# Kernel optimization log

Measured on AMD Instinct MI355X. Metric: run time of the kernel, lower is better.

The kernel has to match this reference:

```python
import jax, jax.numpy as jnp
import numpy as np

BN_EPS = 1e-5


def _conv1x1(x, W, b):
    # x: (B, Cin, H, W), W: (Cout, Cin), b: (Cout,)
    return jnp.einsum('bchw,oc->bohw', x, W) + b[None, :, None, None]


def _bn(x, gamma, beta, mean, var):
    # inference-mode BatchNorm2d with running stats
    inv = gamma / jnp.sqrt(var + BN_EPS)
    return x * inv[None, :, None, None] + (beta - mean * inv)[None, :, None, None]


def setup_inputs() -> dict:
    key = jax.random.key(0)
    ks = jax.random.split(key, 8)
    B, N, C, H, W = 4, 3, 256, 48, 48
    Ck = C // 2  # key/query/value channels (scale=2)
    s = 0.02
    return {
        'x': jax.random.normal(ks[0], (B, N, C, H, W), jnp.float32),
        # f_key / f_query (shared): conv1x1 + BN
        'Wk': jax.random.normal(ks[1], (Ck, C), jnp.float32) * s,
        'bk': jnp.zeros((Ck,), jnp.float32),
        'gk': jnp.ones((Ck,), jnp.float32),
        'betak': jnp.zeros((Ck,), jnp.float32),
        'mk': jnp.zeros((Ck,), jnp.float32),
        'vk': jnp.ones((Ck,), jnp.float32),
        # f_value
        'Wv': jax.random.normal(ks[2], (Ck, C), jnp.float32) * s,
        'bv': jnp.zeros((Ck,), jnp.float32),
        # f_out
        'Wo': jax.random.normal(ks[3], (C, Ck), jnp.float32) * s,
        'bo': jnp.zeros((C,), jnp.float32),
        # fuse_layer: in = 2*C, out = C
        'Wf': jax.random.normal(ks[4], (C, 2 * C), jnp.float32) * s,
        'bf': jnp.zeros((C,), jnp.float32),
    }


def reference(x, Wk, bk, gk, betak, mk, vk, Wv, bv, Wo, bo, Wf, bf):
    B, N, C, H, W = x.shape  # N == 3
    HW = H * W
    Ck = Wk.shape[0]
    scale = Ck ** (-0.5)

    # Precompute shared key/query and value features for all 3 views
    xf = x.reshape(B * N, C, H, W)
    k_all = _bn(_conv1x1(xf, Wk, bk), gk, betak, mk, vk).reshape(B, N, Ck, HW)
    v_all = _conv1x1(xf, Wv, bv).reshape(B, N, Ck, HW)

    outs = []
    attn_maps = []
    for i in range(3):  # fixed small structural loop over views
        adj_ids = [j for j in range(3) if j != i]
        ref = x[:, i]                          # (B, C, H, W)
        q = k_all[:, i].transpose(0, 2, 1)     # (B, HW, Ck)  f_query == f_key
        matching = jnp.zeros_like(ref)
        for j in adj_ids:
            sim = jnp.einsum('bqc,bck->bqk', q, k_all[:, j]) * scale  # (B, HW, HW)
            attn = jax.nn.softmax(sim, axis=-1)
            ctx = jnp.einsum('bqk,bck->bcq', attn, v_all[:, j])       # (B, Ck, HW)
            ctx = ctx.reshape(B, Ck, H, W)
            matching = matching + _conv1x1(ctx, Wo, bo)
            if i == 0:
                attn_maps.append(attn)
        fuse = _conv1x1(jnp.concatenate([ref, matching], axis=1), Wf, bf)
        outs.append(ref + fuse)

    out = jnp.stack(outs, axis=1)                    # (B, 3, C, H, W)
    attention_maps = jnp.stack(attn_maps, axis=1)    # (B, 2, HW, HW)
    return out, attention_maps
```

## Files before the change

kernel.cpp:

```cpp
#include <hip/hip_runtime.h>

typedef short s8v __attribute__((ext_vector_type(8)));
typedef short s4v __attribute__((ext_vector_type(4)));
typedef float f4v __attribute__((ext_vector_type(4)));
typedef unsigned short u16;

#define MFMA(a,b,c) __builtin_amdgcn_mfma_f32_16x16x32_bf16(a,b,c,0,0,0)

__device__ __forceinline__ float bf2f(u16 x){
  unsigned u = ((unsigned)x) << 16;
  return __builtin_bit_cast(float, u);
}
__device__ __forceinline__ u16 f2bf(float f){
  unsigned u = __builtin_bit_cast(unsigned, f);
  u += 0x7FFFu + ((u >> 16) & 1u);
  return (u16)(u >> 16);
}

__device__ __forceinline__ void gload16(const void* g, void* l){
  __builtin_amdgcn_global_load_lds((const __attribute__((address_space(1))) unsigned*)g,
                                   (__attribute__((address_space(3))) unsigned*)l, 16, 0, 0);
}

#define CC   256
#define CK   128
#define HW   2304
#define NF   12
#define OFF_XT   0u
#define OFF_KT   14155776u
#define OFF_V    21233664u
#define OFF_CTX  28311552u
#define OFF_RS   42467328u
#define OFF_PAR  42541056u
#define OFF_WK16 42543104u
#define OFF_WV16 42608640u
#define OFF_WF16 42674176u
#define OFF_WCMB 42936320u

__global__ void cv_weights(const float* __restrict__ Wk, const float* __restrict__ Wv,
                           const float* __restrict__ Wf,
                           u16* __restrict__ Wk16, u16* __restrict__ Wv16, u16* __restrict__ Wf16){
  int i = blockIdx.x*256 + threadIdx.x;
  if (i < 32768){ Wk16[i] = f2bf(Wk[i]); Wv16[i] = f2bf(Wv[i]); }
  Wf16[i] = f2bf(Wf[i]);
}

__global__ void k0_params(const float* __restrict__ bk, const float* __restrict__ gk,
                          const float* __restrict__ betak, const float* __restrict__ mk,
                          const float* __restrict__ vk, const float* __restrict__ Wo,
                          const float* __restrict__ Wf, const float* __restrict__ bo,
                          const float* __restrict__ bfv,
                          float* kscale, float* kbias, float* btot, u16* Wcomb){
  int c = blockIdx.x;
  int o = threadIdx.x;
  float acc = 0.f;
  for(int m=0;m<256;m++)
    acc += Wf[(size_t)o*512 + 256 + m] * Wo[(size_t)m*128 + c];
  Wcomb[(size_t)o*128 + c] = f2bf(acc);
  if (c == 0){
    float a2 = 0.f;
    for(int m=0;m<256;m++)
      a2 += Wf[(size_t)o*512 + 256 + m] * bo[m];
    btot[o] = bfv[o] + 2.0f*a2;
    if (o < 128){
      float inv = gk[o] * rsqrtf(vk[o] + 1e-5f);
      kscale[o] = inv;
      kbias[o]  = betak[o] + (bk[o] - mk[o])*inv;
    }
  }
}

__global__ __launch_bounds__(256) void t0_transpose(const float* __restrict__ x, u16* __restrict__ xT){
  int f = blockIdx.z, cb = blockIdx.y*64, pb = blockIdx.x*64;
  __shared__ u16 tile[64][72];
  int t = threadIdx.x;
  const float* xp = x + (size_t)f*CC*HW;
  int cl = t>>2, pc = (t&3)*8;
  #pragma unroll
  for(int k=0;k<2;k++){
    const float* src = xp + (size_t)(cb+cl)*HW + pb + pc + 32*k;
    f4v v0 = *(const f4v*)(src);
    f4v v1 = *(const f4v*)(src + 4);
    u16* dst = &tile[cl][pc + 32*k];
    #pragma unroll
    for(int u=0;u<4;u++){ dst[u] = f2bf(v0[u]); dst[4+u] = f2bf(v1[u]); }
  }
  __syncthreads();
  u16* xo = xT + (size_t)f*HW*CC;
  int pl = t>>2, cc = (t&3)*8;
  #pragma unroll
  for(int k=0;k<2;k++){
    s8v v;
    #pragma unroll
    for(int u=0;u<8;u++) v[u] = (short)tile[cc + 32*k + u][pl];
    *(s8v*)(xo + (size_t)(pb+pl)*CC + cb + cc + 32*k) = v;
  }
}

__global__ __launch_bounds__(256) void k1_kv(const u16* __restrict__ xT, const u16* __restrict__ Wk,
                                             const u16* __restrict__ Wv, const float* __restrict__ bv,
                                             const float* __restrict__ kscale, const float* __restrict__ kbias,
                                             u16* __restrict__ kT, u16* __restrict__ vout){
  int f  = blockIdx.y;
  int pb = blockIdx.x*64;
  int w = threadIdx.x>>6, l = threadIdx.x&63, s = l&15, g = l>>4;
  const u16* xTf = xT + (size_t)f*HW*CC;
  {
    int q0 = pb + 16*w;
    s8v afr[8];
    #pragma unroll
    for(int kt=0;kt<8;kt++) afr[kt] = *(const s8v*)(xTf + (size_t)(q0+s)*CC + 32*kt + 8*g);
    f4v acc[8] = {};
    #pragma unroll
    for(int kt=0;kt<8;kt++){
      #pragma unroll
      for(int nt=0;nt<8;nt++){
        s8v b = *(const s8v*)(Wk + (size_t)(16*nt+s)*CC + 32*kt + 8*g);
        acc[nt] = MFMA(afr[kt], b, acc[nt]);
      }
    }
    u16* kout = kT + (size_t)f*HW*CK;
    #pragma unroll
    for(int nt=0;nt<8;nt++){
      int o = 16*nt + s;
      float sc = kscale[o], bi = kbias[o];
      #pragma unroll
      for(int r=0;r<4;r++){
        int q = q0 + 4*g + r;
        kout[(size_t)q*CK + o] = f2bf(acc[nt][r]*sc + bi);
      }
    }
  }
  {
    s8v afr[2][8];
    #pragma unroll
    for(int mt=0;mt<2;mt++)
      #pragma unroll
      for(int kt=0;kt<8;kt++)
        afr[mt][kt] = *(const s8v*)(Wv + (size_t)(32*w+16*mt+s)*CC + 32*kt + 8*g);
    f4v acc[2][4] = {};
    #pragma unroll
    for(int kt=0;kt<8;kt++){
      #pragma unroll
      for(int nt=0;nt<4;nt++){
        s8v b = *(const s8v*)(xTf + (size_t)(pb+16*nt+s)*CC + 32*kt + 8*g);
        #pragma unroll
        for(int mt=0;mt<2;mt++)
          acc[mt][nt] = MFMA(afr[mt][kt], b, acc[mt][nt]);
      }
    }
    u16* vf = vout + (size_t)f*CK*HW;
    #pragma unroll
    for(int mt=0;mt<2;mt++){
      #pragma unroll
      for(int r=0;r<4;r++){
        int o = 32*w + 16*mt + 4*g + r;
        float bvo = bv[o];
        #pragma unroll
        for(int nt=0;nt<4;nt++)
          vf[(size_t)o*HW + pb + 16*nt + s] = f2bf(acc[mt][nt][r] + bvo);
      }
    }
  }
}

__global__ __launch_bounds__(256, 2) void k2_attn(const u16* __restrict__ kT, const u16* __restrict__ v,
                                                  u16* __restrict__ ctxS, float* __restrict__ rowsum_ws){
  int qb  = blockIdx.x;
  int bij = blockIdx.y;
  int b = bij/6, r6 = bij - 6*b, i = r6>>1, jj = r6&1;
  int adj0 = (i==0) ? 1 : 0;
  int adj1 = (i==2) ? 1 : 2;
  int j = jj ? adj1 : adj0;
  int tid = threadIdx.x;
  int w = tid>>6, l = tid&63, s = l&15, g = l>>4;
  int q0 = qb*128 + w*32;

  __shared__ char L[81920];
  char* plw = L + 65536 + w*4096;

  const u16* kTi = kT + (size_t)(b*3+i)*HW*CK;
  const u16* kTj = kT + (size_t)(b*3+j)*HW*CK;
  const u16* vj  = v  + (size_t)(b*3+j)*CK*HW;

  s8v qfr[2][4];
  #pragma unroll
  for(int qf=0;qf<2;qf++)
    #pragma unroll
    for(int kt=0;kt<4;kt++)
      qfr[qf][kt] = *(const s8v*)(kTi + (size_t)(q0+16*qf+s)*CK + 32*kt + 8*g);

  const float scale = 0.08838834764831845f;
  f4v ctx[8][2] = {};
  float psum[2][4] = {};

  auto STAGE = [&](int p0, int buf){
    const char* kbase = (const char*)kTj + (size_t)p0*256;
    const char* vbase = (const char*)vj  + (size_t)p0*2;
    char* lK = L + buf*16384 + w*1024;
    char* lV = L + 32768 + buf*16384 + w*1024;
    #pragma unroll
    for(int it=0; it<4; ++it){
      unsigned Lo = (unsigned)tid*16u + (unsigned)it*4096u;
      unsigned Gs = Lo ^ (((Lo>>8)&7u)<<4);
      gload16(kbase + Gs, lK + it*4096);
      unsigned row = Lo>>7;
      unsigned col = (Lo & 127u) ^ ((row&7u)<<4);
      gload16(vbase + (size_t)row*(HW*2) + col, lV + it*4096);
    }
  };

  STAGE(0, 0);
  __syncthreads();
  int cur = 0;

  for(int pt=0; pt<36; ++pt){
    if (pt < 35) STAGE((pt+1)*64, cur^1);
    const char* lK = L + cur*16384;
    const char* lV = L + 32768 + cur*16384;

    f4v sa[2][4] = {};
    #pragma unroll
    for(int kt=0;kt<4;kt++){
      #pragma unroll
      for(int nt=0;nt<4;nt++){
        unsigned row = (unsigned)(16*nt + s);
        unsigned cb  = ((unsigned)(64*kt + 16*g)) ^ ((row&7u)<<4);
        s8v bfr = *(const s8v*)(lK + row*256 + cb);
        #pragma unroll
        for(int qf=0;qf<2;qf++) sa[qf][nt] = MFMA(qfr[qf][kt], bfr, sa[qf][nt]);
      }
    }
    #pragma unroll
    for(int qf=0;qf<2;qf++){
      #pragma unroll
      for(int r=0;r<4;r++){
        unsigned rowr = (unsigned)(4*g + r);
        unsigned rb   = (unsigned)qf*2048u + rowr*128u;
        unsigned swz  = (rowr&7u)<<4;
        #pragma unroll
        for(int nt=0;nt<4;nt++){
          float pv = __expf(sa[qf][nt][r]*scale);
          psum[qf][r] += pv;
          *(u16*)(plw + rb + (((unsigned)(32*nt + 2*s)) ^ swz)) = f2bf(pv);
        }
      }
    }
    s8v pf[2][2];
    #pragma unroll
    for(int qf=0;qf<2;qf++)
      #pragma unroll
      for(int kt=0;kt<2;kt++)
        pf[qf][kt] = *(const s8v*)(plw + (unsigned)qf*2048u + (unsigned)s*128u +
                                   (((unsigned)(64*kt + 16*g)) ^ ((unsigned)(s&7)<<4)));
    #pragma unroll
    for(int kt=0;kt<2;kt++){
      #pragma unroll
      for(int ct=0;ct<8;ct++){
        unsigned row = (unsigned)(16*ct + s);
        unsigned cb  = ((unsigned)(64*kt + 16*g)) ^ ((row&7u)<<4);
        s8v vfr = *(const s8v*)(lV + row*128 + cb);
        #pragma unroll
        for(int qf=0;qf<2;qf++) ctx[ct][qf] = MFMA(vfr, pf[qf][kt], ctx[ct][qf]);
      }
    }
    __syncthreads();
    cur ^= 1;
  }

  #pragma unroll
  for(int qf=0;qf<2;qf++)
    #pragma unroll
    for(int r=0;r<4;r++){
      float x = psum[qf][r];
      x += __shfl_xor(x,1); x += __shfl_xor(x,2); x += __shfl_xor(x,4); x += __shfl_xor(x,8);
      psum[qf][r] = x;
    }
  float* prw = (float*)plw;
  if (s == 0){
    #pragma unroll
    for(int qf=0;qf<2;qf++)
      #pragma unroll
      for(int r=0;r<4;r++) prw[qf*16 + 4*g + r] = psum[qf][r];
  }
  float inv0 = 1.0f / prw[s];
  float inv1 = 1.0f / prw[16 + s];
  if (i == 0 && s == 0){
    #pragma unroll
    for(int qf=0;qf<2;qf++)
      #pragma unroll
      for(int r=0;r<4;r++)
        rowsum_ws[(size_t)(b*2+jj)*HW + q0 + qf*16 + 4*g + r] = psum[qf][r];
  }
  u16* cS = ctxS + (size_t)bij*HW*CK;
  #pragma unroll
  for(int qf=0;qf<2;qf++){
    float inv = qf ? inv1 : inv0;
    #pragma unroll
    for(int ct=0;ct<8;ct++){
      s4v pk;
      #pragma unroll
      for(int r=0;r<4;r++) pk[r] = (short)f2bf(ctx[ct][qf][r]*inv);
      *(s4v*)(cS + (size_t)(q0+qf*16+s)*CK + 16*ct + 4*g) = pk;
    }
  }
}

__global__ __launch_bounds__(256) void k2c_attnmap(const u16* __restrict__ kT,
                                                   const float* __restrict__ rowsum_ws,
                                                   float* __restrict__ attn_out){
  int qb = blockIdx.x;
  int y  = blockIdx.y;
  int plane = y>>1, ph = y&1;
  int b = plane>>1, jj = plane&1, j = jj + 1;
  int tid = threadIdx.x;
  int w = tid>>6, l = tid&63, s = l&15, g = l>>4;
  int q0 = qb*64 + w*16;

  __shared__ char  ldsK[16384];
  __shared__ float ptile[4][16][68];
  __shared__ float inv16[4][16];

  const u16* kTi = kT + (size_t)(b*3)*HW*CK;
  const u16* kTj = kT + (size_t)(b*3+j)*HW*CK;

  s8v qf[4];
  #pragma unroll
  for(int kt=0;kt<4;kt++) qf[kt] = *(const s8v*)(kTi + (size_t)(q0+s)*CK + 32*kt + 8*g);

  {
    f4v rsv = *(const f4v*)(rowsum_ws + (size_t)plane*HW + q0 + 4*g);
    if (s == 0){
      #pragma unroll
      for(int r=0;r<4;r++) inv16[w][4*g+r] = 1.0f / rsv[r];
    }
  }
  __syncthreads();

  const float scale = 0.08838834764831845f;
  float* ao = attn_out + (size_t)plane*HW*HW;

  for(int pt=ph*18; pt<ph*18+18; ++pt){
    int p0 = pt*64;
    {
      const char* kbase = (const char*)kTj + (size_t)p0*256;
      char* lK = (char*)ldsK + w*1024;
      #pragma unroll
      for(int it=0; it<4; ++it){
        unsigned Lo = (unsigned)tid*16u + (unsigned)it*4096u;
        unsigned Gs = Lo ^ (((Lo>>8)&7u)<<4);
        gload16(kbase + Gs, lK + it*4096);
      }
    }
    __syncthreads();

    f4v sa[4] = {};
    #pragma unroll
    for(int kt=0;kt<4;kt++){
      #pragma unroll
      for(int nt=0;nt<4;nt++){
        unsigned row = (unsigned)(16*nt + s);
        unsigned cb  = ((unsigned)(64*kt + 16*g)) ^ ((row&7u)<<4);
        s8v bfr = *(const s8v*)((const char*)ldsK + row*256 + cb);
        sa[nt] = MFMA(qf[kt], bfr, sa[nt]);
      }
    }
    #pragma unroll
    for(int r=0;r<4;r++){
      #pragma unroll
      for(int nt=0;nt<4;nt++)
        ptile[w][4*g+r][16*nt+s] = __expf(sa[nt][r]*scale);
    }
    #pragma unroll
    for(int pass=0; pass<4; ++pass){
      int row = 4*pass + g;
      float inv = inv16[w][row];
      f4v val = *(const f4v*)&ptile[w][row][4*s];
      #pragma unroll
      for(int u=0;u<4;u++) val[u] *= inv;
      *(f4v*)(ao + (size_t)(q0+row)*HW + p0 + 4*s) = val;
    }
    __syncthreads();
  }
}

__global__ __launch_bounds__(256) void k3_out(const float* __restrict__ x, const u16* __restrict__ xT,
                                              const u16* __restrict__ Wf, const u16* __restrict__ Wcomb,
                                              const float* __restrict__ btot, const u16* __restrict__ ctxS,
                                              float* __restrict__ out){
  int f = blockIdx.y, pb = blockIdx.x*64;
  int w = threadIdx.x>>6, l = threadIdx.x&63, s = l&15, g = l>>4;
  const u16* xTf = xT + (size_t)f*HW*CC;
  const u16* cS0 = ctxS + (size_t)(f*2+0)*HW*CK;
  const u16* cS1 = ctxS + (size_t)(f*2+1)*HW*CK;
  f4v acc[4][4] = {};
  #pragma unroll
  for(int kt=0;kt<8;kt++){
    s8v bfr[4];
    #pragma unroll
    for(int nt=0;nt<4;nt++) bfr[nt] = *(const s8v*)(xTf + (size_t)(pb+16*nt+s)*CC + 32*kt + 8*g);
    #pragma unroll
    for(int mt=0;mt<4;mt++){
      s8v a = *(const s8v*)(Wf + (size_t)(64*w+16*mt+s)*512 + 32*kt + 8*g);
      #pragma unroll
      for(int nt=0;nt<4;nt++) acc[mt][nt] = MFMA(a, bfr[nt], acc[mt][nt]);
    }
  }
  #pragma unroll
  for(int kt=0;kt<4;kt++){
    s8v b0[4], b1[4];
    #pragma unroll
    for(int nt=0;nt<4;nt++){
      b0[nt] = *(const s8v*)(cS0 + (size_t)(pb+16*nt+s)*CK + 32*kt + 8*g);
      b1[nt] = *(const s8v*)(cS1 + (size_t)(pb+16*nt+s)*CK + 32*kt + 8*g);
    }
    #pragma unroll
    for(int mt=0;mt<4;mt++){
      s8v a = *(const s8v*)(Wcomb + (size_t)(64*w+16*mt+s)*CK + 32*kt + 8*g);
      #pragma unroll
      for(int nt=0;nt<4;nt++){
        acc[mt][nt] = MFMA(a, b0[nt], acc[mt][nt]);
        acc[mt][nt] = MFMA(a, b1[nt], acc[mt][nt]);
      }
    }
  }
  const float* xf = x + (size_t)f*CC*HW;
  float* of = out + (size_t)f*CC*HW;
  #pragma unroll
  for(int mt=0;mt<4;mt++){
    #pragma unroll
    for(int r=0;r<4;r++){
      int o = 64*w + 16*mt + 4*g + r;
      float bb = btot[o];
      #pragma unroll
      for(int nt=0;nt<4;nt++){
        int p = pb + 16*nt + s;
        of[(size_t)o*HW + p] = acc[mt][nt][r] + bb + xf[(size_t)o*HW + p];
      }
    }
  }
}

extern "C" void kernel_launch(void* const* d_in, const int* in_sizes, int n_in,
                              void* d_out, int out_size, void* d_ws, size_t ws_size,
                              hipStream_t stream) {
  const float* x     = (const float*)d_in[0];
  const float* Wk    = (const float*)d_in[1];
  const float* bk    = (const float*)d_in[2];
  const float* gk    = (const float*)d_in[3];
  const float* betak = (const float*)d_in[4];
  const float* mk    = (const float*)d_in[5];
  const float* vk    = (const float*)d_in[6];
  const float* Wv    = (const float*)d_in[7];
  const float* bv    = (const float*)d_in[8];
  const float* Wo    = (const float*)d_in[9];
  const float* bo    = (const float*)d_in[10];
  const float* Wf    = (const float*)d_in[11];
  const float* bf    = (const float*)d_in[12];
  float* out = (float*)d_out;

  char* ws = (char*)d_ws;
  u16*   xT     = (u16*)(ws + OFF_XT);
  u16*   kT     = (u16*)(ws + OFF_KT);
  u16*   vv     = (u16*)(ws + OFF_V);
  u16*   ctxS   = (u16*)(ws + OFF_CTX);
  float* rs     = (float*)(ws + OFF_RS);
  float* kscale = (float*)(ws + OFF_PAR);
  float* kbias  = kscale + 128;
  float* btot   = kbias + 128;
  u16*   Wk16   = (u16*)(ws + OFF_WK16);
  u16*   Wv16   = (u16*)(ws + OFF_WV16);
  u16*   Wf16   = (u16*)(ws + OFF_WF16);
  u16*   Wcomb  = (u16*)(ws + OFF_WCMB);

  float* attn = out + (size_t)NF*CC*HW;

  cv_weights<<<dim3(512), dim3(256), 0, stream>>>(Wk, Wv, Wf, Wk16, Wv16, Wf16);
  k0_params<<<dim3(128), dim3(256), 0, stream>>>(bk, gk, betak, mk, vk, Wo, Wf, bo, bf,
                                                 kscale, kbias, btot, Wcomb);
  t0_transpose<<<dim3(36,4,12), dim3(256), 0, stream>>>(x, xT);
  k1_kv<<<dim3(36,12), dim3(256), 0, stream>>>(xT, Wk16, Wv16, bv, kscale, kbias, kT, vv);
  k2_attn<<<dim3(18,24), dim3(256), 0, stream>>>(kT, vv, ctxS, rs);
  k2c_attnmap<<<dim3(36,16), dim3(256), 0, stream>>>(kT, rs, attn);
  k3_out<<<dim3(36,12), dim3(256), 0, stream>>>(x, xT, Wf16, Wcomb, btot, ctxS, out);
}
```

Before: 244.9 us.

## Fuse x transpose into consumers and slim attention kernel LDS and softmax

Removes the standalone transpose kernel and the bf16 xT buffer. k1_kv and k3_out now each convert their own 64-pixel slab of x into swizzled shared memory. In k2_attn, V is read directly from global memory instead of being staged in LDS, which cuts shared memory from 80 KB to 48 KB so launch bounds can allow 3 blocks per SM. The QK MFMA operands are swapped so each lane holds a full row for the softmax, making the row-sum reduction a 2-step shuffle with packed P stores. exp is switched to exp2f with a folded scale. The costs are that x is read and converted twice (once in k1, once in k3) and V loads now go uncached-through-LDS from global.

```diff
diff --git a/kernel.cpp b/kernel.cpp
--- a/kernel.cpp
+++ b/kernel.cpp
@@ -3,6 +3,7 @@
 typedef short s8v __attribute__((ext_vector_type(8)));
 typedef short s4v __attribute__((ext_vector_type(4)));
 typedef float f4v __attribute__((ext_vector_type(4)));
+typedef unsigned u32v2 __attribute__((ext_vector_type(2)));
 typedef unsigned short u16;
 
 #define MFMA(a,b,c) __builtin_amdgcn_mfma_f32_16x16x32_bf16(a,b,c,0,0,0)
@@ -26,7 +27,7 @@
 #define CK   128
 #define HW   2304
 #define NF   12
-#define OFF_XT   0u
+#define C2E  0.1275174996992022f
 #define OFF_KT   14155776u
 #define OFF_V    21233664u
 #define OFF_CTX  28311552u
@@ -70,46 +71,38 @@
   }
 }
 
-__global__ __launch_bounds__(256) void t0_transpose(const float* __restrict__ x, u16* __restrict__ xT){
-  int f = blockIdx.z, cb = blockIdx.y*64, pb = blockIdx.x*64;
-  __shared__ u16 tile[64][72];
-  int t = threadIdx.x;
-  const float* xp = x + (size_t)f*CC*HW;
-  int cl = t>>2, pc = (t&3)*8;
-  #pragma unroll
-  for(int k=0;k<2;k++){
-    const float* src = xp + (size_t)(cb+cl)*HW + pb + pc + 32*k;
-    f4v v0 = *(const f4v*)(src);
-    f4v v1 = *(const f4v*)(src + 4);
-    u16* dst = &tile[cl][pc + 32*k];
-    #pragma unroll
-    for(int u=0;u<4;u++){ dst[u] = f2bf(v0[u]); dst[4+u] = f2bf(v1[u]); }
-  }
-  __syncthreads();
-  u16* xo = xT + (size_t)f*HW*CC;
-  int pl = t>>2, cc = (t&3)*8;
-  #pragma unroll
-  for(int k=0;k<2;k++){
-    s8v v;
-    #pragma unroll
-    for(int u=0;u<8;u++) v[u] = (short)tile[cc + 32*k + u][pl];
-    *(s8v*)(xo + (size_t)(pb+pl)*CC + cb + cc + 32*k) = v;
-  }
-}
-
-__global__ __launch_bounds__(256) void k1_kv(const u16* __restrict__ xT, const u16* __restrict__ Wk,
+__device__ __forceinline__ void stage_xt(const float* __restrict__ xf, int pb, int tid, char* xt){
+  #pragma unroll
+  for(int it=0; it<16; ++it){
+    int idx = tid + 256*it;
+    int c = idx>>4, slot = idx&15;
+    f4v v = *(const f4v*)(xf + (size_t)c*HW + pb + slot*4);
+    #pragma unroll
+    for(int u=0;u<4;u++){
+      int p = slot*4+u;
+      *(u16*)(xt + p*512 + ((2*c) ^ ((p&7)<<4))) = f2bf(v[u]);
+    }
+  }
+}
+__device__ __forceinline__ s8v xt_frag(const char* xt, int r, int kt, int g){
+  return *(const s8v*)(xt + r*512 + (((unsigned)(64*kt+16*g)) ^ ((unsigned)(r&7)<<4)));
+}
+
+__global__ __launch_bounds__(256) void k1_kv(const float* __restrict__ x, const u16* __restrict__ Wk,
                                              const u16* __restrict__ Wv, const float* __restrict__ bv,
                                              const float* __restrict__ kscale, const float* __restrict__ kbias,
                                              u16* __restrict__ kT, u16* __restrict__ vout){
   int f  = blockIdx.y;
   int pb = blockIdx.x*64;
-  int w = threadIdx.x>>6, l = threadIdx.x&63, s = l&15, g = l>>4;
-  const u16* xTf = xT + (size_t)f*HW*CC;
+  int tid = threadIdx.x;
+  int w = tid>>6, l = tid&63, s = l&15, g = l>>4;
+  __shared__ char xt[32768];
+  stage_xt(x + (size_t)f*CC*HW, pb, tid, xt);
+  __syncthreads();
   {
-    int q0 = pb + 16*w;
     s8v afr[8];
     #pragma unroll
-    for(int kt=0;kt<8;kt++) afr[kt] = *(const s8v*)(xTf + (size_t)(q0+s)*CC + 32*kt + 8*g);
+    for(int kt=0;kt<8;kt++) afr[kt] = xt_frag(xt, 16*w+s, kt, g);
     f4v acc[8] = {};
     #pragma unroll
     for(int kt=0;kt<8;kt++){
@@ -120,6 +113,7 @@
       }
     }
     u16* kout = kT + (size_t)f*HW*CK;
+    int q0 = pb + 16*w;
     #pragma unroll
     for(int nt=0;nt<8;nt++){
       int o = 16*nt + s;
@@ -143,7 +137,7 @@
     for(int kt=0;kt<8;kt++){
       #pragma unroll
       for(int nt=0;nt<4;nt++){
-        s8v b = *(const s8v*)(xTf + (size_t)(pb+16*nt+s)*CC + 32*kt + 8*g);
+        s8v b = xt_frag(xt, 16*nt+s, kt, g);
         #pragma unroll
         for(int mt=0;mt<2;mt++)
           acc[mt][nt] = MFMA(afr[mt][kt], b, acc[mt][nt]);
@@ -164,7 +158,7 @@
   }
 }
 
-__global__ __launch_bounds__(256, 2) void k2_attn(const u16* __restrict__ kT, const u16* __restrict__ v,
+__global__ __launch_bounds__(256, 3) void k2_attn(const u16* __restrict__ kT, const u16* __restrict__ v,
                                                   u16* __restrict__ ctxS, float* __restrict__ rowsum_ws){
   int qb  = blockIdx.x;
   int bij = blockIdx.y;
@@ -176,8 +170,8 @@
   int w = tid>>6, l = tid&63, s = l&15, g = l>>4;
   int q0 = qb*128 + w*32;
 
-  __shared__ char L[81920];
-  char* plw = L + 65536 + w*4096;
+  __shared__ char L[49152];
+  char* plw = L + 32768 + w*4096;
 
   const u16* kTi = kT + (size_t)(b*3+i)*HW*CK;
   const u16* kTj = kT + (size_t)(b*3+j)*HW*CK;
@@ -190,23 +184,17 @@
     for(int kt=0;kt<4;kt++)
       qfr[qf][kt] = *(const s8v*)(kTi + (size_t)(q0+16*qf+s)*CK + 32*kt + 8*g);
 
-  const float scale = 0.08838834764831845f;
   f4v ctx[8][2] = {};
-  float psum[2][4] = {};
+  float psum[2] = {0.f, 0.f};
 
   auto STAGE = [&](int p0, int buf){
     const char* kbase = (const char*)kTj + (size_t)p0*256;
-    const char* vbase = (const char*)vj  + (size_t)p0*2;
     char* lK = L + buf*16384 + w*1024;
-    char* lV = L + 32768 + buf*16384 + w*1024;
     #pragma unroll
     for(int it=0; it<4; ++it){
       unsigned Lo = (unsigned)tid*16u + (unsigned)it*4096u;
       unsigned Gs = Lo ^ (((Lo>>8)&7u)<<4);
       gload16(kbase + Gs, lK + it*4096);
-      unsigned row = Lo>>7;
-      unsigned col = (Lo & 127u) ^ ((row&7u)<<4);
-      gload16(vbase + (size_t)row*(HW*2) + col, lV + it*4096);
     }
   };
 
@@ -215,9 +203,9 @@
   int cur = 0;
 
   for(int pt=0; pt<36; ++pt){
-    if (pt < 35) STAGE((pt+1)*64, cur^1);
+    int p0 = pt*64;
+    if (pt < 35) STAGE(p0+64, cur^1);
     const char* lK = L + cur*16384;
-    const char* lV = L + 32768 + cur*16384;
 
     f4v sa[2][4] = {};
     #pragma unroll
@@ -226,24 +214,25 @@
       for(int nt=0;nt<4;nt++){
         unsigned row = (unsigned)(16*nt + s);
         unsigned cb  = ((unsigned)(64*kt + 16*g)) ^ ((row&7u)<<4);
-        s8v bfr = *(const s8v*)(lK + row*256 + cb);
+        s8v kfr = *(const s8v*)(lK + row*256 + cb);
         #pragma unroll
-        for(int qf=0;qf<2;qf++) sa[qf][nt] = MFMA(qfr[qf][kt], bfr, sa[qf][nt]);
+        for(int qf=0;qf<2;qf++) sa[qf][nt] = MFMA(kfr, qfr[qf][kt], sa[qf][nt]);
       }
     }
     #pragma unroll
     for(int qf=0;qf<2;qf++){
       #pragma unroll
-      for(int r=0;r<4;r++){
-        unsigned rowr = (unsigned)(4*g + r);
-        unsigned rb   = (unsigned)qf*2048u + rowr*128u;
-        unsigned swz  = (rowr&7u)<<4;
-        #pragma unroll
-        for(int nt=0;nt<4;nt++){
-          float pv = __expf(sa[qf][nt][r]*scale);
-          psum[qf][r] += pv;
-          *(u16*)(plw + rb + (((unsigned)(32*nt + 2*s)) ^ swz)) = f2bf(pv);
-        }
+      for(int nt=0;nt<4;nt++){
+        float e0 = exp2f(sa[qf][nt][0]*C2E);
+        float e1 = exp2f(sa[qf][nt][1]*C2E);
+        float e2 = exp2f(sa[qf][nt][2]*C2E);
+        float e3 = exp2f(sa[qf][nt][3]*C2E);
+        psum[qf] += (e0+e1)+(e2+e3);
+        u32v2 pk;
+        pk[0] = (unsigned)f2bf(e0) | ((unsigned)f2bf(e1)<<16);
+        pk[1] = (unsigned)f2bf(e2) | ((unsigned)f2bf(e3)<<16);
+        unsigned off = ((unsigned)(32*nt + 8*g)) ^ ((unsigned)(s&7)<<4);
+        *(u32v2*)(plw + (unsigned)qf*2048u + (unsigned)s*128u + off) = pk;
       }
     }
     s8v pf[2][2];
@@ -257,9 +246,7 @@
     for(int kt=0;kt<2;kt++){
       #pragma unroll
       for(int ct=0;ct<8;ct++){
-        unsigned row = (unsigned)(16*ct + s);
-        unsigned cb  = ((unsigned)(64*kt + 16*g)) ^ ((row&7u)<<4);
-        s8v vfr = *(const s8v*)(lV + row*128 + cb);
+        s8v vfr = *(const s8v*)(vj + (size_t)(16*ct+s)*HW + p0 + 32*kt + 8*g);
         #pragma unroll
         for(int qf=0;qf<2;qf++) ctx[ct][qf] = MFMA(vfr, pf[qf][kt], ctx[ct][qf]);
       }
@@ -268,40 +255,25 @@
     cur ^= 1;
   }
 
-  #pragma unroll
-  for(int qf=0;qf<2;qf++)
-    #pragma unroll
-    for(int r=0;r<4;r++){
-      float x = psum[qf][r];
-      x += __shfl_xor(x,1); x += __shfl_xor(x,2); x += __shfl_xor(x,4); x += __shfl_xor(x,8);
-      psum[qf][r] = x;
-    }
-  float* prw = (float*)plw;
-  if (s == 0){
-    #pragma unroll
-    for(int qf=0;qf<2;qf++)
-      #pragma unroll
-      for(int r=0;r<4;r++) prw[qf*16 + 4*g + r] = psum[qf][r];
-  }
-  float inv0 = 1.0f / prw[s];
-  float inv1 = 1.0f / prw[16 + s];
-  if (i == 0 && s == 0){
-    #pragma unroll
-    for(int qf=0;qf<2;qf++)
-      #pragma unroll
-      for(int r=0;r<4;r++)
-        rowsum_ws[(size_t)(b*2+jj)*HW + q0 + qf*16 + 4*g + r] = psum[qf][r];
+  float inv[2];
+  #pragma unroll
+  for(int qf=0;qf<2;qf++){
+    float xsum = psum[qf];
+    xsum += __shfl_xor(xsum, 16);
+    xsum += __shfl_xor(xsum, 32);
+    inv[qf] = 1.0f / xsum;
+    if (i == 0 && l < 16)
+      rowsum_ws[(size_t)(b*2+jj)*HW + q0 + 16*qf + s] = xsum;
   }
   u16* cS = ctxS + (size_t)bij*HW*CK;
   #pragma unroll
   for(int qf=0;qf<2;qf++){
-    float inv = qf ? inv1 : inv0;
     #pragma unroll
     for(int ct=0;ct<8;ct++){
       s4v pk;
       #pragma unroll
-      for(int r=0;r<4;r++) pk[r] = (short)f2bf(ctx[ct][qf][r]*inv);
-      *(s4v*)(cS + (size_t)(q0+qf*16+s)*CK + 16*ct + 4*g) = pk;
+      for(int r=0;r<4;r++) pk[r] = (short)f2bf(ctx[ct][qf][r]*inv[qf]);
+      *(s4v*)(cS + (size_t)(q0+16*qf+s)*CK + 16*ct + 4*g) = pk;
     }
   }
 }
@@ -337,7 +309,6 @@
   }
   __syncthreads();
 
-  const float scale = 0.08838834764831845f;
   float* ao = attn_out + (size_t)plane*HW*HW;
 
   for(int pt=ph*18; pt<ph*18+18; ++pt){
@@ -369,7 +340,7 @@
     for(int r=0;r<4;r++){
       #pragma unroll
       for(int nt=0;nt<4;nt++)
-        ptile[w][4*g+r][16*nt+s] = __expf(sa[nt][r]*scale);
+        ptile[w][4*g+r][16*nt+s] = exp2f(sa[nt][r]*C2E);
     }
     #pragma unroll
     for(int pass=0; pass<4; ++pass){
@@ -384,13 +355,17 @@
   }
 }
 
-__global__ __launch_bounds__(256) void k3_out(const float* __restrict__ x, const u16* __restrict__ xT,
+__global__ __launch_bounds__(256) void k3_out(const float* __restrict__ x,
                                               const u16* __restrict__ Wf, const u16* __restrict__ Wcomb,
                                               const float* __restrict__ btot, const u16* __restrict__ ctxS,
                                               float* __restrict__ out){
   int f = blockIdx.y, pb = blockIdx.x*64;
-  int w = threadIdx.x>>6, l = threadIdx.x&63, s = l&15, g = l>>4;
-  const u16* xTf = xT + (size_t)f*HW*CC;
+  int tid = threadIdx.x;
+  int w = tid>>6, l = tid&63, s = l&15, g = l>>4;
+  __shared__ char xt[32768];
+  const float* xf = x + (size_t)f*CC*HW;
+  stage_xt(xf, pb, tid, xt);
+  __syncthreads();
   const u16* cS0 = ctxS + (size_t)(f*2+0)*HW*CK;
   const u16* cS1 = ctxS + (size_t)(f*2+1)*HW*CK;
   f4v acc[4][4] = {};
@@ -398,7 +373,7 @@
   for(int kt=0;kt<8;kt++){
     s8v bfr[4];
     #pragma unroll
-    for(int nt=0;nt<4;nt++) bfr[nt] = *(const s8v*)(xTf + (size_t)(pb+16*nt+s)*CC + 32*kt + 8*g);
+    for(int nt=0;nt<4;nt++) bfr[nt] = xt_frag(xt, 16*nt+s, kt, g);
     #pragma unroll
     for(int mt=0;mt<4;mt++){
       s8v a = *(const s8v*)(Wf + (size_t)(64*w+16*mt+s)*512 + 32*kt + 8*g);
@@ -424,7 +399,6 @@
       }
     }
   }
-  const float* xf = x + (size_t)f*CC*HW;
   float* of = out + (size_t)f*CC*HW;
   #pragma unroll
   for(int mt=0;mt<4;mt++){
@@ -460,7 +434,6 @@
   float* out = (float*)d_out;
 
   char* ws = (char*)d_ws;
-  u16*   xT     = (u16*)(ws + OFF_XT);
   u16*   kT     = (u16*)(ws + OFF_KT);
   u16*   vv     = (u16*)(ws + OFF_V);
   u16*   ctxS   = (u16*)(ws + OFF_CTX);
@@ -478,9 +451,8 @@
   cv_weights<<<dim3(512), dim3(256), 0, stream>>>(Wk, Wv, Wf, Wk16, Wv16, Wf16);
   k0_params<<<dim3(128), dim3(256), 0, stream>>>(bk, gk, betak, mk, vk, Wo, Wf, bo, bf,
                                                  kscale, kbias, btot, Wcomb);
-  t0_transpose<<<dim3(36,4,12), dim3(256), 0, stream>>>(x, xT);
-  k1_kv<<<dim3(36,12), dim3(256), 0, stream>>>(xT, Wk16, Wv16, bv, kscale, kbias, kT, vv);
+  k1_kv<<<dim3(36,12), dim3(256), 0, stream>>>(x, Wk16, Wv16, bv, kscale, kbias, kT, vv);
   k2_attn<<<dim3(18,24), dim3(256), 0, stream>>>(kT, vv, ctxS, rs);
   k2c_attnmap<<<dim3(36,16), dim3(256), 0, stream>>>(kT, rs, attn);
-  k3_out<<<dim3(36,12), dim3(256), 0, stream>>>(x, xT, Wf16, Wcomb, btot, ctxS, out);
-}
+  k3_out<<<dim3(36,12), dim3(256), 0, stream>>>(x, Wf16, Wcomb, btot, ctxS, out);
+}
```

After: 373.9 us. 52.7% more time.
